# Kernel optimization log

Measured on AMD Instinct MI355X. Metric: run time of the kernel, lower is better.

## Reference

```python
import jax, jax.numpy as jnp
import numpy as np

B, N, F, U = 16, 2048, 64, 64

def setup_inputs() -> dict:
    key = jax.random.key(0)
    k1, k2, k3 = jax.random.split(key, 3)
    node_features = jax.random.normal(k1, (B, N, F), dtype=jnp.float32)
    adjacency_matrix = (jax.random.uniform(k2, (B, N, N)) < 0.01).astype(jnp.float32)
    kernel = jax.random.normal(k3, (F, U), dtype=jnp.float32) * (1.0 / np.sqrt(F))
    return {"node_features": node_features, "adjacency_matrix": adjacency_matrix, "kernel": kernel}

def reference(node_features, adjacency_matrix, kernel):
    # A_tilde = A + I  (self-loops)
    n = adjacency_matrix.shape[-1]
    adj = adjacency_matrix + jnp.eye(n, dtype=adjacency_matrix.dtype)
    # symmetric normalization D^-1/2 A_tilde D^-1/2 (diag matmuls == broadcast scaling)
    row_sum = jnp.sum(adj, axis=-1)                      # [B, N]
    d_inv_sqrt = jnp.where(row_sum > 0, row_sum ** -0.5, 0.0)
    norm_adj = d_inv_sqrt[:, :, None] * adj * d_inv_sqrt[:, None, :]
    # feature transform then aggregate, fused with ReLU
    transformed = jnp.einsum('bnf,fu->bnu', node_features, kernel)
    out = jnp.einsum('bnm,bmu->bnu', norm_adj, transformed)
    return jax.nn.relu(out)
```

## Files before the change

### kernel.cpp

```cpp
#include <hip/hip_runtime.h>
#include <hip/hip_bf16.h>


#define NB     16
#define NN     2048
#define NF     64
#define NU     64
#define NROWS  (NB * NN)

__global__ __launch_bounds__(256) void k1_rowsum_compact(
    const float* __restrict__ A, float* __restrict__ d,
    int* __restrict__ counts, int2* __restrict__ pairs, int cap)
{
    const int row = blockIdx.x;
    const float* Arow = A + (size_t)row * NN;
    __shared__ int   s_cnt;
    __shared__ float s_part[4];
    if (threadIdx.x == 0) s_cnt = 0;
    __syncthreads();

    const int t = threadIdx.x;
    const size_t base = (size_t)row * cap;
    float sum = 0.f;
    #pragma unroll
    for (int k = 0; k < 2; ++k) {
        const int i4 = t + k * 256;
        const float4 a = reinterpret_cast<const float4*>(Arow)[i4];
        const float v[4] = {a.x, a.y, a.z, a.w};
        #pragma unroll
        for (int c = 0; c < 4; ++c) {
            if (v[c] != 0.f) {
                sum += v[c];
                const int slot = atomicAdd(&s_cnt, 1);
                if (slot < cap) {
                    int2 e; e.x = i4 * 4 + c; e.y = __float_as_int(v[c]);
                    pairs[base + slot] = e;
                }
            }
        }
    }
    #pragma unroll
    for (int o = 32; o > 0; o >>= 1) sum += __shfl_down(sum, o);
    const int wid = t >> 6, lane = t & 63;
    if (lane == 0) s_part[wid] = sum;
    __syncthreads();
    if (t == 0) {
        const float tot = s_part[0] + s_part[1] + s_part[2] + s_part[3] + 1.0f;
        d[row]      = rsqrtf(tot);
        counts[row] = s_cnt;
    }
}

__global__ __launch_bounds__(256) void k2_transform_scale(
    const float* __restrict__ X, const float* __restrict__ W,
    const float* __restrict__ d, float* __restrict__ Tp)
{
    __shared__ float sW[NF * NU];
    const int t = threadIdx.x;
    for (int k = t; k < NF * NU; k += 256) sW[k] = W[k];
    __syncthreads();

    const int wid = t >> 6, lane = t & 63;
    const int row = blockIdx.x * 4 + wid;
    const float* Xr = X + (size_t)row * NF;
    float acc = 0.f;
    #pragma unroll
    for (int f = 0; f < NF; ++f) acc += Xr[f] * sW[f * NU + lane];
    Tp[(size_t)row * NU + lane] = acc * d[row];
}

__global__ __launch_bounds__(256) void k3_aggregate(
    const float* __restrict__ A, const float* __restrict__ Tp,
    const float* __restrict__ d, const int* __restrict__ counts,
    const int2* __restrict__ pairs, float* __restrict__ out, int cap)
{
    const int t = threadIdx.x;
    const int wid = t >> 6, lane = t & 63;
    const int row = blockIdx.x * 4 + wid;
    const int b   = row >> 11;
    const float* Tb = Tp + (((size_t)b) << 11) * NU;

    float acc = Tp[(size_t)row * NU + lane];
    const int cnt = counts[row];
    if (cnt <= cap) {
        const size_t base = (size_t)row * cap;
        for (int k = 0; k < cnt; ++k) {
            const int2 e = pairs[base + k];
            acc += __int_as_float(e.y) * Tb[((size_t)e.x << 6) + lane];
        }
    } else {
        const float* Arow = A + (size_t)row * NN;
        for (int j = 0; j < NN; ++j) {
            const float v = Arow[j];
            if (v != 0.f) acc += v * Tb[((size_t)j << 6) + lane];
        }
    }
    const float r = d[row] * acc;
    out[(size_t)row * NU + lane] = r > 0.f ? r : 0.f;
}

extern "C" void kernel_launch(void* const* d_in, const int* in_sizes, int n_in,
                              void* d_out, int out_size, void* d_ws, size_t ws_size,
                              hipStream_t stream)
{
    const float* X = (const float*)d_in[0];
    const float* A = (const float*)d_in[1];
    const float* W = (const float*)d_in[2];
    float* out = (float*)d_out;

    char* ws = (char*)d_ws;
    float* Tp     = (float*)ws;
    float* dvec   = (float*)(ws + (size_t)NROWS * NU * 4);
    int*   counts = (int*)  (ws + (size_t)NROWS * NU * 4 + NROWS * 4);
    int2*  pairs  = (int2*) (ws + (size_t)NROWS * NU * 4 + 2ull * NROWS * 4);

    const size_t fixed = (size_t)NROWS * NU * 4 + 2ull * NROWS * 4;
    int cap = 0;
    if (ws_size > fixed) {
        size_t c = (ws_size - fixed) / ((size_t)NROWS * sizeof(int2));
        cap = (int)(c < 128 ? c : 128);
    }

    k1_rowsum_compact<<<NROWS, 256, 0, stream>>>(A, dvec, counts, pairs, cap);
    k2_transform_scale<<<NROWS / 4, 256, 0, stream>>>(X, W, dvec, Tp);
    k3_aggregate<<<NROWS / 4, 256, 0, stream>>>(A, Tp, dvec, counts, pairs, out, cap);
}
```

Before: 445.2 us.

## Use wave-ballot compaction, register-resident weights, and vectorized pair loads

```diff
diff --git a/kernel.cpp b/kernel.cpp
--- a/kernel.cpp
+++ b/kernel.cpp
@@ -7,6 +7,8 @@
 #define NF     64
 #define NU     64
 #define NROWS  (NB * NN)
+
+typedef float vfloat4 __attribute__((ext_vector_type(4)));
 
 __global__ __launch_bounds__(256) void k1_rowsum_compact(
     const float* __restrict__ A, float* __restrict__ d,
@@ -20,28 +22,38 @@
     __syncthreads();
 
     const int t = threadIdx.x;
+    const int lane = t & 63;
     const size_t base = (size_t)row * cap;
+    const unsigned long long lmask_lt = (lane == 63) ? 0x7fffffffffffffffull
+                                                     : ((1ull << lane) - 1ull);
     float sum = 0.f;
     #pragma unroll
     for (int k = 0; k < 2; ++k) {
         const int i4 = t + k * 256;
-        const float4 a = reinterpret_cast<const float4*>(Arow)[i4];
-        const float v[4] = {a.x, a.y, a.z, a.w};
+        const vfloat4 a = __builtin_nontemporal_load(
+            reinterpret_cast<const vfloat4*>(Arow) + i4);
         #pragma unroll
         for (int c = 0; c < 4; ++c) {
-            if (v[c] != 0.f) {
-                sum += v[c];
-                const int slot = atomicAdd(&s_cnt, 1);
-                if (slot < cap) {
-                    int2 e; e.x = i4 * 4 + c; e.y = __float_as_int(v[c]);
-                    pairs[base + slot] = e;
+            const float vv = a[c];
+            sum += vv;
+            const unsigned long long m = __ballot(vv != 0.f);
+            if (m) {
+                int wb = 0;
+                if (lane == 0) wb = atomicAdd(&s_cnt, __popcll(m));
+                wb = __shfl(wb, 0);
+                if (vv != 0.f) {
+                    const int slot = wb + __popcll(m & lmask_lt);
+                    if (slot < cap) {
+                        int2 e; e.x = i4 * 4 + c; e.y = __float_as_int(vv);
+                        pairs[base + slot] = e;
+                    }
                 }
             }
         }
     }
     #pragma unroll
     for (int o = 32; o > 0; o >>= 1) sum += __shfl_down(sum, o);
-    const int wid = t >> 6, lane = t & 63;
+    const int wid = t >> 6;
     if (lane == 0) s_part[wid] = sum;
     __syncthreads();
     if (t == 0) {
@@ -55,18 +67,21 @@
     const float* __restrict__ X, const float* __restrict__ W,
     const float* __restrict__ d, float* __restrict__ Tp)
 {
-    __shared__ float sW[NF * NU];
     const int t = threadIdx.x;
-    for (int k = t; k < NF * NU; k += 256) sW[k] = W[k];
-    __syncthreads();
+    const int lane = t & 63;
+    float wcol[NF];
+    #pragma unroll
+    for (int f = 0; f < NF; ++f) wcol[f] = W[f * NU + lane];
 
-    const int wid = t >> 6, lane = t & 63;
-    const int row = blockIdx.x * 4 + wid;
-    const float* Xr = X + (size_t)row * NF;
-    float acc = 0.f;
-    #pragma unroll
-    for (int f = 0; f < NF; ++f) acc += Xr[f] * sW[f * NU + lane];
-    Tp[(size_t)row * NU + lane] = acc * d[row];
+    const int wave_gid = (blockIdx.x * 256 + t) >> 6;
+    const int n_waves  = (gridDim.x * 256) >> 6;
+    for (int row = wave_gid; row < NROWS; row += n_waves) {
+        const float xv = X[(size_t)row * NF + lane];
+        float acc = 0.f;
+        #pragma unroll
+        for (int f = 0; f < NF; ++f) acc += __shfl(xv, f) * wcol[f];
+        Tp[(size_t)row * NU + lane] = acc * d[row];
+    }
 }
 
 __global__ __launch_bounds__(256) void k3_aggregate(
@@ -84,7 +99,21 @@
     const int cnt = counts[row];
     if (cnt <= cap) {
         const size_t base = (size_t)row * cap;
-        for (int k = 0; k < cnt; ++k) {
+        const int4* p4 = reinterpret_cast<const int4*>(pairs + base);
+        int k = 0;
+        for (; k + 4 <= cnt; k += 4) {
+            const int4 q0 = p4[k >> 1];
+            const int4 q1 = p4[(k >> 1) + 1];
+            const float t0 = Tb[((size_t)q0.x << 6) + lane];
+            const float t1 = Tb[((size_t)q0.z << 6) + lane];
+            const float t2 = Tb[((size_t)q1.x << 6) + lane];
+            const float t3 = Tb[((size_t)q1.z << 6) + lane];
+            acc += __int_as_float(q0.y) * t0;
+            acc += __int_as_float(q0.w) * t1;
+            acc += __int_as_float(q1.y) * t2;
+            acc += __int_as_float(q1.w) * t3;
+        }
+        for (; k < cnt; ++k) {
             const int2 e = pairs[base + k];
             acc += __int_as_float(e.y) * Tb[((size_t)e.x << 6) + lane];
         }
@@ -111,7 +140,7 @@
     char* ws = (char*)d_ws;
     float* Tp     = (float*)ws;
     float* dvec   = (float*)(ws + (size_t)NROWS * NU * 4);
-    int*   counts = (int*)  (ws + (size_t)NROWS * NU * 4 + NROWS * 4);
+    int*   counts = (int*)  (ws + (size_t)NROWS * NU * 4 + (size_t)NROWS * 4);
     int2*  pairs  = (int2*) (ws + (size_t)NROWS * NU * 4 + 2ull * NROWS * 4);
 
     const size_t fixed = (size_t)NROWS * NU * 4 + 2ull * NROWS * 4;
@@ -119,9 +148,10 @@
     if (ws_size > fixed) {
         size_t c = (ws_size - fixed) / ((size_t)NROWS * sizeof(int2));
         cap = (int)(c < 128 ? c : 128);
+        cap &= ~1;
     }
 
     k1_rowsum_compact<<<NROWS, 256, 0, stream>>>(A, dvec, counts, pairs, cap);
-    k2_transform_scale<<<NROWS / 4, 256, 0, stream>>>(X, W, dvec, Tp);
+    k2_transform_scale<<<1024, 256, 0, stream>>>(X, W, dvec, Tp);
     k3_aggregate<<<NROWS / 4, 256, 0, stream>>>(A, Tp, dvec, counts, pairs, out, cap);
 }
```

New measurement: 404.3 us. 1.1x faster.
